# Optimization experiments

Measured on AMD Instinct MI355X. Metric: run time of the kernel, lower is better.

The kernel has to match this reference:

```python
import jax, jax.numpy as jnp
import numpy as np

GROUP_SIZE = 128  # in_features // scales.shape[1]


def setup_inputs() -> dict:
    key = jax.random.key(0)
    kA, kq, ks, kz, kb = jax.random.split(key, 5)
    M, K, N = 2048, 4096, 4096
    G = K // GROUP_SIZE  # 32 groups
    A = jax.random.normal(kA, (M, K), dtype=jnp.float32)
    # unpacked uint4 quantized weights, values in [0, 16)
    qweight = jax.random.randint(kq, (N, K), 0, 16, dtype=jnp.int32)
    # per-group scales (typical GPTQ magnitude) and zero-points (float, 'original' zeros_mode)
    scales = jax.random.uniform(ks, (N, G), dtype=jnp.float32) * 0.02
    zeros = jax.random.uniform(kz, (N, G), dtype=jnp.float32) * 15.0
    bias = jax.random.normal(kb, (N,), dtype=jnp.float32)
    return {"A": A, "qweight": qweight, "scales": scales, "zeros": zeros, "bias": bias}


def reference(A, qweight, scales, zeros, bias):
    # Dequant: W[n,k] = (q[n,k] - zeros[n, k//gs]) * scales[n, k//gs]
    N, K = qweight.shape
    gs = K // scales.shape[1]
    s = jnp.repeat(scales, gs, axis=1)  # [N, K]
    z = jnp.repeat(zeros, gs, axis=1)   # [N, K]
    W = (qweight.astype(A.dtype) - z) * s
    # out[m,n] = sum_k A[m,k] * W[n,k] + bias[n]
    return jnp.einsum("mk,nk->mn", A, W) + bias
```

## Files before the change

### kernel.cpp

```cpp
#include <hip/hip_runtime.h>
#include <cstdint>
#include <cstddef>

#define MM 2048
#define KK 4096
#define NN 4096
#define GG 32
#define BM 128
#define BN 128
#define BK 64

typedef _Float16 half8_t __attribute__((ext_vector_type(8)));
typedef _Float16 half4_t __attribute__((ext_vector_type(4)));
typedef float f32x4 __attribute__((ext_vector_type(4)));

__device__ __forceinline__ void load_lds16(const void* gptr, void* lptr) {
  __builtin_amdgcn_global_load_lds(
      (const __attribute__((address_space(1))) unsigned int*)gptr,
      (__attribute__((address_space(3))) unsigned int*)lptr, 16, 0, 0);
}

#define ACNT (MM * KK / 4)
__global__ void prep_kernel(const float* __restrict__ A, const int* __restrict__ q,
                            const float* __restrict__ scales, const float* __restrict__ zeros,
                            _Float16* __restrict__ Ah, _Float16* __restrict__ Wh) {
  const int i = blockIdx.x * blockDim.x + threadIdx.x;
  if (i < ACNT) {
    const float4 v = ((const float4*)A)[i];
    half4_t h;
    h[0] = (_Float16)v.x; h[1] = (_Float16)v.y; h[2] = (_Float16)v.z; h[3] = (_Float16)v.w;
    *(half4_t*)(Ah + 4 * (size_t)i) = h;
  } else {
    const int j = i - ACNT;
    const int e = j << 2;
    const int n = e >> 12;
    const int k = e & (KK - 1);
    const int g = k >> 7;
    const float sc = scales[(n << 5) + g];
    const float zp = zeros[(n << 5) + g];
    const float nzs = -zp * sc;
    const int4 qv = ((const int4*)q)[j];
    half4_t h;
    h[0] = (_Float16)fmaf((float)qv.x, sc, nzs);
    h[1] = (_Float16)fmaf((float)qv.y, sc, nzs);
    h[2] = (_Float16)fmaf((float)qv.z, sc, nzs);
    h[3] = (_Float16)fmaf((float)qv.w, sc, nzs);
    *(half4_t*)(Wh + (size_t)e) = h;
  }
}

template <bool FUSED>
__global__ __launch_bounds__(256, 2)
void gemm_kernel(const _Float16* __restrict__ Ah, const _Float16* __restrict__ Wh,
                 const float* __restrict__ Af, const int* __restrict__ qw,
                 const float* __restrict__ scales, const float* __restrict__ zeros,
                 const float* __restrict__ bias, float* __restrict__ out)
{
  __shared__ __align__(16) _Float16 sA[BM * BK];
  __shared__ __align__(16) _Float16 sB[BN * BK];

  const int tid = threadIdx.x;
  const int lane = tid & 63;
  const int wave = tid >> 6;
  const int wr = wave >> 1, wc = wave & 1;

  const int bid = blockIdx.x;
  const int xcd = bid & 7;
  const int slot = bid >> 3;
  const int mt = slot >> 2;
  const int nt = xcd * 4 + (slot & 3);
  const int m0 = mt * BM;
  const int n0 = nt * BN;

  const int lr = lane & 15, quad = lane >> 4;

  f32x4 acc[4][4];
#pragma unroll
  for (int i = 0; i < 4; ++i)
#pragma unroll
    for (int j = 0; j < 4; ++j) acc[i][j] = (f32x4){0.f, 0.f, 0.f, 0.f};

  const int srow = lane >> 3;
  const int scc = lane & 7;
  const int gchunk = scc ^ srow;

  const int frow = tid >> 4;
  const int fc4 = tid & 15;

  for (int kt = 0; kt < KK / BK; ++kt) {
    const int k0 = kt * BK;
    if constexpr (!FUSED) {
#pragma unroll
      for (int i = 0; i < 4; ++i) {
        const int c = i * 4 + wave;
        const int row = c * 8 + srow;
        load_lds16(Ah + (size_t)(m0 + row) * KK + k0 + gchunk * 8, (void*)&sA[c * 512]);
        load_lds16(Wh + (size_t)(n0 + row) * KK + k0 + gchunk * 8, (void*)&sB[c * 512]);
      }
    } else {
      const int g = k0 >> 7;
#pragma unroll
      for (int p = 0; p < 8; ++p) {
        const int row = p * 16 + frow;
        const int pc = (fc4 >> 1) ^ (row & 7);
        const int dst = row * 64 + pc * 8 + (fc4 & 1) * 4;
        const float4 avf = *(const float4*)&Af[(size_t)(m0 + row) * KK + k0 + fc4 * 4];
        half4_t ah;
        ah[0] = (_Float16)avf.x; ah[1] = (_Float16)avf.y;
        ah[2] = (_Float16)avf.z; ah[3] = (_Float16)avf.w;
        *(half4_t*)&sA[dst] = ah;
        const int n = n0 + row;
        const float sc = scales[(n << 5) + g];
        const float zp = zeros[(n << 5) + g];
        const float nzs = -zp * sc;
        const int4 qv = *(const int4*)&qw[(size_t)n * KK + k0 + fc4 * 4];
        half4_t bh;
        bh[0] = (_Float16)fmaf((float)qv.x, sc, nzs);
        bh[1] = (_Float16)fmaf((float)qv.y, sc, nzs);
        bh[2] = (_Float16)fmaf((float)qv.z, sc, nzs);
        bh[3] = (_Float16)fmaf((float)qv.w, sc, nzs);
        *(half4_t*)&sB[dst] = bh;
      }
    }
    __syncthreads();
#pragma unroll
    for (int ks = 0; ks < 2; ++ks) {
      half8_t a[4], b[4];
#pragma unroll
      for (int t = 0; t < 4; ++t) {
        const int rA = wr * 64 + t * 16 + lr;
        const int j = ks * 4 + quad;
        a[t] = *(const half8_t*)&sA[rA * 64 + ((j ^ (lr & 7)) * 8)];
        const int rB = wc * 64 + t * 16 + lr;
        b[t] = *(const half8_t*)&sB[rB * 64 + ((j ^ (lr & 7)) * 8)];
      }
#pragma unroll
      for (int mi = 0; mi < 4; ++mi)
#pragma unroll
        for (int ni = 0; ni < 4; ++ni)
          acc[mi][ni] = __builtin_amdgcn_mfma_f32_16x16x32_f16(a[mi], b[ni], acc[mi][ni], 0, 0, 0);
    }
    __syncthreads();
  }

#pragma unroll
  for (int ni = 0; ni < 4; ++ni) {
    const int n = n0 + wc * 64 + ni * 16 + lr;
    const float bv = bias[n];
#pragma unroll
    for (int mi = 0; mi < 4; ++mi) {
      const int mbase = m0 + wr * 64 + mi * 16 + quad * 4;
#pragma unroll
      for (int r = 0; r < 4; ++r)
        out[(size_t)(mbase + r) * NN + n] = acc[mi][ni][r] + bv;
    }
  }
}

extern "C" void kernel_launch(void* const* d_in, const int* in_sizes, int n_in,
                              void* d_out, int out_size, void* d_ws, size_t ws_size,
                              hipStream_t stream) {
  (void)in_sizes; (void)n_in; (void)out_size;
  const float* A      = (const float*)d_in[0];
  const int*   qw     = (const int*)d_in[1];
  const float* scales = (const float*)d_in[2];
  const float* zeros  = (const float*)d_in[3];
  const float* bias   = (const float*)d_in[4];
  float* out = (float*)d_out;

  const size_t needA = (size_t)MM * KK * sizeof(_Float16);
  const size_t needW = (size_t)NN * KK * sizeof(_Float16);

  dim3 grid(NN / BN * MM / BM);
  dim3 block(256);

  if (ws_size >= needA + needW) {
    _Float16* Ah = (_Float16*)d_ws;
    _Float16* Wh = (_Float16*)((char*)d_ws + needA);
    prep_kernel<<<((MM + NN) * KK / 4) / 256, 256, 0, stream>>>(A, qw, scales, zeros, Ah, Wh);
    gemm_kernel<false><<<grid, block, 0, stream>>>(Ah, Wh, A, qw, scales, zeros, bias, out);
  } else {
    gemm_kernel<true><<<grid, block, 0, stream>>>(nullptr, nullptr, A, qw, scales, zeros, bias, out);
  }
}
```

Measured before the change: 204.6 us.

## Add triple-buffered 8-wave GEMM with 128x256 tiles and interleaved LDS prefetch

Replaces the workspace GEMM path with a 512-thread, 8-wave kernel using 128x256 tiles and a three-stage LDS ring. Async global-to-LDS loads for tile t+2 are issued between the fragment reads and the MFMA phases, with explicit vmcnt waits, barriers and setprio, so memory traffic overlaps compute. The prep kernel also processes 8 elements per thread. The larger tiles cut redundant A/W reloads but raise LDS use (about 144KB per block) and register pressure, which may limit occupancy.

Result: no change. 207.7 us (+1.5%).

```diff
diff --git a/kernel.cpp b/kernel.cpp
--- a/kernel.cpp
+++ b/kernel.cpp
@@ -7,8 +7,9 @@
 #define NN 4096
 #define GG 32
 #define BM 128
-#define BN 128
+#define BN 256
 #define BK 64
+#define NTILES (KK / BK)
 
 typedef _Float16 half8_t __attribute__((ext_vector_type(8)));
 typedef _Float16 half4_t __attribute__((ext_vector_type(4)));
@@ -20,44 +21,170 @@
       (__attribute__((address_space(3))) unsigned int*)lptr, 16, 0, 0);
 }
 
-#define ACNT (MM * KK / 4)
+#define ACNT8 (MM * KK / 8)
 __global__ void prep_kernel(const float* __restrict__ A, const int* __restrict__ q,
                             const float* __restrict__ scales, const float* __restrict__ zeros,
                             _Float16* __restrict__ Ah, _Float16* __restrict__ Wh) {
   const int i = blockIdx.x * blockDim.x + threadIdx.x;
-  if (i < ACNT) {
-    const float4 v = ((const float4*)A)[i];
-    half4_t h;
-    h[0] = (_Float16)v.x; h[1] = (_Float16)v.y; h[2] = (_Float16)v.z; h[3] = (_Float16)v.w;
-    *(half4_t*)(Ah + 4 * (size_t)i) = h;
+  if (i < ACNT8) {
+    const float4 v0 = ((const float4*)A)[2 * (size_t)i];
+    const float4 v1 = ((const float4*)A)[2 * (size_t)i + 1];
+    half8_t h;
+    h[0] = (_Float16)v0.x; h[1] = (_Float16)v0.y; h[2] = (_Float16)v0.z; h[3] = (_Float16)v0.w;
+    h[4] = (_Float16)v1.x; h[5] = (_Float16)v1.y; h[6] = (_Float16)v1.z; h[7] = (_Float16)v1.w;
+    *(half8_t*)(Ah + 8 * (size_t)i) = h;
   } else {
-    const int j = i - ACNT;
-    const int e = j << 2;
+    const int j = i - ACNT8;
+    const int e = j << 3;
     const int n = e >> 12;
     const int k = e & (KK - 1);
     const int g = k >> 7;
     const float sc = scales[(n << 5) + g];
     const float zp = zeros[(n << 5) + g];
     const float nzs = -zp * sc;
-    const int4 qv = ((const int4*)q)[j];
-    half4_t h;
-    h[0] = (_Float16)fmaf((float)qv.x, sc, nzs);
-    h[1] = (_Float16)fmaf((float)qv.y, sc, nzs);
-    h[2] = (_Float16)fmaf((float)qv.z, sc, nzs);
-    h[3] = (_Float16)fmaf((float)qv.w, sc, nzs);
-    *(half4_t*)(Wh + (size_t)e) = h;
-  }
-}
-
-template <bool FUSED>
+    const int4 q0 = ((const int4*)q)[2 * (size_t)j];
+    const int4 q1 = ((const int4*)q)[2 * (size_t)j + 1];
+    half8_t h;
+    h[0] = (_Float16)fmaf((float)q0.x, sc, nzs);
+    h[1] = (_Float16)fmaf((float)q0.y, sc, nzs);
+    h[2] = (_Float16)fmaf((float)q0.z, sc, nzs);
+    h[3] = (_Float16)fmaf((float)q0.w, sc, nzs);
+    h[4] = (_Float16)fmaf((float)q1.x, sc, nzs);
+    h[5] = (_Float16)fmaf((float)q1.y, sc, nzs);
+    h[6] = (_Float16)fmaf((float)q1.z, sc, nzs);
+    h[7] = (_Float16)fmaf((float)q1.w, sc, nzs);
+    *(half8_t*)(Wh + (size_t)e) = h;
+  }
+}
+
+__global__ __launch_bounds__(512, 2)
+void gemm8_kernel(const _Float16* __restrict__ Ah, const _Float16* __restrict__ Wh,
+                  const float* __restrict__ bias, float* __restrict__ out)
+{
+  __shared__ __align__(16) _Float16 sA[3][BM * BK];
+  __shared__ __align__(16) _Float16 sB[3][BN * BK];
+
+  const int tid = threadIdx.x;
+  const int lane = tid & 63;
+  const int wave = tid >> 6;
+  const int wr = wave >> 2;
+  const int wc = wave & 3;
+  const int lr = lane & 15, quad = lane >> 4;
+
+  const int bid = blockIdx.x;
+  const int xcd = bid & 7;
+  const int slot = bid >> 3;
+  const int mt = slot >> 1;
+  const int nt = xcd * 2 + (slot & 1);
+  const int m0 = mt * BM;
+  const int n0 = nt * BN;
+
+  const int srow = lane >> 3, scc = lane & 7, gch = scc ^ srow;
+
+  f32x4 acc[4][4];
+#pragma unroll
+  for (int i = 0; i < 4; ++i)
+#pragma unroll
+    for (int j = 0; j < 4; ++j) acc[i][j] = (f32x4){0.f, 0.f, 0.f, 0.f};
+
+  auto stageA = [&](int t, int buf, int i) {
+    load_lds16(Ah + (size_t)(m0 + i * 64 + (wave << 3) + srow) * KK + t * BK + (gch << 3),
+               (void*)&sA[buf][(i * 64 + (wave << 3)) * BK]);
+  };
+  auto stageB = [&](int t, int buf, int i) {
+    load_lds16(Wh + (size_t)(n0 + i * 64 + (wave << 3) + srow) * KK + t * BK + (gch << 3),
+               (void*)&sB[buf][(i * 64 + (wave << 3)) * BK]);
+  };
+
+  stageB(0, 0, 0); stageB(0, 0, 1); stageA(0, 0, 0);
+  stageB(0, 0, 2); stageB(0, 0, 3); stageA(0, 0, 1);
+  stageB(1, 1, 0); stageB(1, 1, 1); stageA(1, 1, 0);
+  stageB(1, 1, 2); stageB(1, 1, 3); stageA(1, 1, 1);
+  asm volatile("s_waitcnt vmcnt(6)" ::: "memory");
+  __builtin_amdgcn_s_barrier();
+
+  int cur = 0, nb = 2;
+  for (int t = 0; t < NTILES; ++t) {
+    const _Float16* pA = sA[cur];
+    const _Float16* pB = sB[cur];
+    const bool st = (t < NTILES - 2);
+    half8_t a0[2][2], a1[2][2], b[4][2];
+
+#pragma unroll
+    for (int x = 0; x < 2; ++x) {
+      const _Float16* ba = &pA[(wr * 64 + x * 16 + lr) * BK];
+#pragma unroll
+      for (int ks = 0; ks < 2; ++ks)
+        a0[x][ks] = *(const half8_t*)&ba[((ks * 4 + quad) ^ (lr & 7)) * 8];
+    }
+#pragma unroll
+    for (int ni = 0; ni < 4; ++ni) {
+      const _Float16* bb = &pB[(wc * 64 + ni * 16 + lr) * BK];
+#pragma unroll
+      for (int ks = 0; ks < 2; ++ks)
+        b[ni][ks] = *(const half8_t*)&bb[((ks * 4 + quad) ^ (lr & 7)) * 8];
+    }
+    if (st) { stageB(t + 2, nb, 0); stageB(t + 2, nb, 1); stageA(t + 2, nb, 0); }
+    __builtin_amdgcn_sched_barrier(0);
+    __builtin_amdgcn_s_barrier();
+    __builtin_amdgcn_s_setprio(1);
+#pragma unroll
+    for (int x = 0; x < 2; ++x)
+#pragma unroll
+      for (int ni = 0; ni < 4; ++ni) {
+        acc[x][ni] = __builtin_amdgcn_mfma_f32_16x16x32_f16(a0[x][0], b[ni][0], acc[x][ni], 0, 0, 0);
+        acc[x][ni] = __builtin_amdgcn_mfma_f32_16x16x32_f16(a0[x][1], b[ni][1], acc[x][ni], 0, 0, 0);
+      }
+    __builtin_amdgcn_s_setprio(0);
+    __builtin_amdgcn_s_barrier();
+
+#pragma unroll
+    for (int x = 0; x < 2; ++x) {
+      const _Float16* ba = &pA[(wr * 64 + (x + 2) * 16 + lr) * BK];
+#pragma unroll
+      for (int ks = 0; ks < 2; ++ks)
+        a1[x][ks] = *(const half8_t*)&ba[((ks * 4 + quad) ^ (lr & 7)) * 8];
+    }
+    if (st) { stageB(t + 2, nb, 2); stageB(t + 2, nb, 3); stageA(t + 2, nb, 1); }
+    __builtin_amdgcn_sched_barrier(0);
+    __builtin_amdgcn_s_barrier();
+    __builtin_amdgcn_s_setprio(1);
+#pragma unroll
+    for (int x = 0; x < 2; ++x)
+#pragma unroll
+      for (int ni = 0; ni < 4; ++ni) {
+        acc[x + 2][ni] = __builtin_amdgcn_mfma_f32_16x16x32_f16(a1[x][0], b[ni][0], acc[x + 2][ni], 0, 0, 0);
+        acc[x + 2][ni] = __builtin_amdgcn_mfma_f32_16x16x32_f16(a1[x][1], b[ni][1], acc[x + 2][ni], 0, 0, 0);
+      }
+    __builtin_amdgcn_s_setprio(0);
+    if (t < NTILES - 2) asm volatile("s_waitcnt vmcnt(6)" ::: "memory");
+    else                asm volatile("s_waitcnt vmcnt(0)" ::: "memory");
+    __builtin_amdgcn_s_barrier();
+    cur = (cur == 2) ? 0 : cur + 1;
+    nb  = (nb  == 2) ? 0 : nb + 1;
+  }
+
+#pragma unroll
+  for (int ni = 0; ni < 4; ++ni) {
+    const int n = n0 + wc * 64 + ni * 16 + lr;
+    const float bv = bias[n];
+#pragma unroll
+    for (int mi = 0; mi < 4; ++mi) {
+      const int mbase = m0 + wr * 64 + mi * 16 + quad * 4;
+#pragma unroll
+      for (int r = 0; r < 4; ++r)
+        out[(size_t)(mbase + r) * NN + n] = acc[mi][ni][r] + bv;
+    }
+  }
+}
+
 __global__ __launch_bounds__(256, 2)
-void gemm_kernel(const _Float16* __restrict__ Ah, const _Float16* __restrict__ Wh,
-                 const float* __restrict__ Af, const int* __restrict__ qw,
-                 const float* __restrict__ scales, const float* __restrict__ zeros,
-                 const float* __restrict__ bias, float* __restrict__ out)
+void gemm_fused_kernel(const float* __restrict__ Af, const int* __restrict__ qw,
+                       const float* __restrict__ scales, const float* __restrict__ zeros,
+                       const float* __restrict__ bias, float* __restrict__ out)
 {
-  __shared__ __align__(16) _Float16 sA[BM * BK];
-  __shared__ __align__(16) _Float16 sB[BN * BK];
+  __shared__ __align__(16) _Float16 sA[128 * 64];
+  __shared__ __align__(16) _Float16 sB[128 * 64];
 
   const int tid = threadIdx.x;
   const int lane = tid & 63;
@@ -69,8 +196,8 @@
   const int slot = bid >> 3;
   const int mt = slot >> 2;
   const int nt = xcd * 4 + (slot & 3);
-  const int m0 = mt * BM;
-  const int n0 = nt * BN;
+  const int m0 = mt * 128;
+  const int n0 = nt * 128;
 
   const int lr = lane & 15, quad = lane >> 4;
 
@@ -79,48 +206,34 @@
   for (int i = 0; i < 4; ++i)
 #pragma unroll
     for (int j = 0; j < 4; ++j) acc[i][j] = (f32x4){0.f, 0.f, 0.f, 0.f};
-
-  const int srow = lane >> 3;
-  const int scc = lane & 7;
-  const int gchunk = scc ^ srow;
 
   const int frow = tid >> 4;
   const int fc4 = tid & 15;
 
-  for (int kt = 0; kt < KK / BK; ++kt) {
-    const int k0 = kt * BK;
-    if constexpr (!FUSED) {
-#pragma unroll
-      for (int i = 0; i < 4; ++i) {
-        const int c = i * 4 + wave;
-        const int row = c * 8 + srow;
-        load_lds16(Ah + (size_t)(m0 + row) * KK + k0 + gchunk * 8, (void*)&sA[c * 512]);
-        load_lds16(Wh + (size_t)(n0 + row) * KK + k0 + gchunk * 8, (void*)&sB[c * 512]);
-      }
-    } else {
-      const int g = k0 >> 7;
-#pragma unroll
-      for (int p = 0; p < 8; ++p) {
-        const int row = p * 16 + frow;
-        const int pc = (fc4 >> 1) ^ (row & 7);
-        const int dst = row * 64 + pc * 8 + (fc4 & 1) * 4;
-        const float4 avf = *(const float4*)&Af[(size_t)(m0 + row) * KK + k0 + fc4 * 4];
-        half4_t ah;
-        ah[0] = (_Float16)avf.x; ah[1] = (_Float16)avf.y;
-        ah[2] = (_Float16)avf.z; ah[3] = (_Float16)avf.w;
-        *(half4_t*)&sA[dst] = ah;
-        const int n = n0 + row;
-        const float sc = scales[(n << 5) + g];
-        const float zp = zeros[(n << 5) + g];
-        const float nzs = -zp * sc;
-        const int4 qv = *(const int4*)&qw[(size_t)n * KK + k0 + fc4 * 4];
-        half4_t bh;
-        bh[0] = (_Float16)fmaf((float)qv.x, sc, nzs);
-        bh[1] = (_Float16)fmaf((float)qv.y, sc, nzs);
-        bh[2] = (_Float16)fmaf((float)qv.z, sc, nzs);
-        bh[3] = (_Float16)fmaf((float)qv.w, sc, nzs);
-        *(half4_t*)&sB[dst] = bh;
-      }
+  for (int kt = 0; kt < KK / 64; ++kt) {
+    const int k0 = kt * 64;
+    const int g = k0 >> 7;
+#pragma unroll
+    for (int p = 0; p < 8; ++p) {
+      const int row = p * 16 + frow;
+      const int pc = (fc4 >> 1) ^ (row & 7);
+      const int dst = row * 64 + pc * 8 + (fc4 & 1) * 4;
+      const float4 avf = *(const float4*)&Af[(size_t)(m0 + row) * KK + k0 + fc4 * 4];
+      half4_t ah;
+      ah[0] = (_Float16)avf.x; ah[1] = (_Float16)avf.y;
+      ah[2] = (_Float16)avf.z; ah[3] = (_Float16)avf.w;
+      *(half4_t*)&sA[dst] = ah;
+      const int n = n0 + row;
+      const float sc = scales[(n << 5) + g];
+      const float zp = zeros[(n << 5) + g];
+      const float nzs = -zp * sc;
+      const int4 qv = *(const int4*)&qw[(size_t)n * KK + k0 + fc4 * 4];
+      half4_t bh;
+      bh[0] = (_Float16)fmaf((float)qv.x, sc, nzs);
+      bh[1] = (_Float16)fmaf((float)qv.y, sc, nzs);
+      bh[2] = (_Float16)fmaf((float)qv.z, sc, nzs);
+      bh[3] = (_Float16)fmaf((float)qv.w, sc, nzs);
+      *(half4_t*)&sB[dst] = bh;
     }
     __syncthreads();
 #pragma unroll
@@ -171,15 +284,12 @@
   const size_t needA = (size_t)MM * KK * sizeof(_Float16);
   const size_t needW = (size_t)NN * KK * sizeof(_Float16);
 
-  dim3 grid(NN / BN * MM / BM);
-  dim3 block(256);
-
   if (ws_size >= needA + needW) {
     _Float16* Ah = (_Float16*)d_ws;
     _Float16* Wh = (_Float16*)((char*)d_ws + needA);
-    prep_kernel<<<((MM + NN) * KK / 4) / 256, 256, 0, stream>>>(A, qw, scales, zeros, Ah, Wh);
-    gemm_kernel<false><<<grid, block, 0, stream>>>(Ah, Wh, A, qw, scales, zeros, bias, out);
+    prep_kernel<<<((MM + NN) * KK / 8) / 256, 256, 0, stream>>>(A, qw, scales, zeros, Ah, Wh);
+    gemm8_kernel<<<dim3(MM / BM * NN / BN), dim3(512), 0, stream>>>(Ah, Wh, bias, out);
   } else {
-    gemm_kernel<true><<<grid, block, 0, stream>>>(nullptr, nullptr, A, qw, scales, zeros, bias, out);
-  }
-}
+    gemm_fused_kernel<<<dim3(512), dim3(256), 0, stream>>>(A, qw, scales, zeros, bias, out);
+  }
+}
```

## Fuse dequant and fp32 conversion into a pipelined 128x256 triple-buffered GEMM

Applied to the files above, without the earlier changes.

Removes the separate prep kernel that wrote fp16 copies of A and W, and instead loads fp32 A and int32 weights directly into registers two tiles ahead. They are converted to fp16 and dequantized while being written into a triple-buffered LDS ring. The block tile grows to 128x256 with 512 threads and a single barrier per K tile, and MFMA issue is prioritized with setprio. This trades the extra HBM round trip of the prep pass for higher per-block global read volume of fp32/int32 data, plus heavy register and LDS usage (about 144KB).

Result: slower. 384.2 us (+87.7%).

```diff
diff --git a/kernel.cpp b/kernel.cpp
--- a/kernel.cpp
+++ b/kernel.cpp
@@ -7,72 +7,41 @@
 #define NN 4096
 #define GG 32
 #define BM 128
-#define BN 128
+#define BN 256
 #define BK 64
+#define NTILES (KK / BK)
 
 typedef _Float16 half8_t __attribute__((ext_vector_type(8)));
-typedef _Float16 half4_t __attribute__((ext_vector_type(4)));
 typedef float f32x4 __attribute__((ext_vector_type(4)));
 
-__device__ __forceinline__ void load_lds16(const void* gptr, void* lptr) {
-  __builtin_amdgcn_global_load_lds(
-      (const __attribute__((address_space(1))) unsigned int*)gptr,
-      (__attribute__((address_space(3))) unsigned int*)lptr, 16, 0, 0);
-}
-
-#define ACNT (MM * KK / 4)
-__global__ void prep_kernel(const float* __restrict__ A, const int* __restrict__ q,
-                            const float* __restrict__ scales, const float* __restrict__ zeros,
-                            _Float16* __restrict__ Ah, _Float16* __restrict__ Wh) {
-  const int i = blockIdx.x * blockDim.x + threadIdx.x;
-  if (i < ACNT) {
-    const float4 v = ((const float4*)A)[i];
-    half4_t h;
-    h[0] = (_Float16)v.x; h[1] = (_Float16)v.y; h[2] = (_Float16)v.z; h[3] = (_Float16)v.w;
-    *(half4_t*)(Ah + 4 * (size_t)i) = h;
-  } else {
-    const int j = i - ACNT;
-    const int e = j << 2;
-    const int n = e >> 12;
-    const int k = e & (KK - 1);
-    const int g = k >> 7;
-    const float sc = scales[(n << 5) + g];
-    const float zp = zeros[(n << 5) + g];
-    const float nzs = -zp * sc;
-    const int4 qv = ((const int4*)q)[j];
-    half4_t h;
-    h[0] = (_Float16)fmaf((float)qv.x, sc, nzs);
-    h[1] = (_Float16)fmaf((float)qv.y, sc, nzs);
-    h[2] = (_Float16)fmaf((float)qv.z, sc, nzs);
-    h[3] = (_Float16)fmaf((float)qv.w, sc, nzs);
-    *(half4_t*)(Wh + (size_t)e) = h;
-  }
-}
-
-template <bool FUSED>
-__global__ __launch_bounds__(256, 2)
-void gemm_kernel(const _Float16* __restrict__ Ah, const _Float16* __restrict__ Wh,
-                 const float* __restrict__ Af, const int* __restrict__ qw,
-                 const float* __restrict__ scales, const float* __restrict__ zeros,
-                 const float* __restrict__ bias, float* __restrict__ out)
+__global__ __launch_bounds__(512, 2)
+void gemm_fused13(const float* __restrict__ Af, const int* __restrict__ qw,
+                  const float* __restrict__ scales, const float* __restrict__ zeros,
+                  const float* __restrict__ bias, float* __restrict__ out)
 {
-  __shared__ __align__(16) _Float16 sA[BM * BK];
-  __shared__ __align__(16) _Float16 sB[BN * BK];
+  __shared__ __align__(16) _Float16 sA[3][BM * BK];
+  __shared__ __align__(16) _Float16 sB[3][BN * BK];
 
   const int tid = threadIdx.x;
   const int lane = tid & 63;
   const int wave = tid >> 6;
-  const int wr = wave >> 1, wc = wave & 1;
+  const int wr = wave >> 2;
+  const int wc = wave & 3;
+  const int lr = lane & 15, quad = lane >> 4;
 
   const int bid = blockIdx.x;
   const int xcd = bid & 7;
   const int slot = bid >> 3;
-  const int mt = slot >> 2;
-  const int nt = xcd * 4 + (slot & 3);
+  const int mt = slot >> 1;
+  const int nt = xcd * 2 + (slot & 1);
   const int m0 = mt * BM;
   const int n0 = nt * BN;
 
-  const int lr = lane & 15, quad = lane >> 4;
+  const int arow = tid >> 2, aquad = tid & 3;
+  const int brow = tid >> 1, bhalf = tid & 1;
+  const size_t aBase = (size_t)(m0 + arow) * KK;
+  const size_t bBase = (size_t)(n0 + brow) * KK;
+  const int szBase = (n0 + brow) << 5;
 
   f32x4 acc[4][4];
 #pragma unroll
@@ -80,68 +49,113 @@
 #pragma unroll
     for (int j = 0; j < 4; ++j) acc[i][j] = (f32x4){0.f, 0.f, 0.f, 0.f};
 
-  const int srow = lane >> 3;
-  const int scc = lane & 7;
-  const int gchunk = scc ^ srow;
+  float4 aR0[4], aR1[4];
+  int4   bR0[8], bR1[8];
+  float  sc0, nz0, sc1, nz1;
 
-  const int frow = tid >> 4;
-  const int fc4 = tid & 15;
+#define LOADSET(T, aR, bR, scR, nzR)                                            \
+  do {                                                                          \
+    const int k0_ = (T) * BK;                                                   \
+    _Pragma("unroll")                                                           \
+    for (int j = 0; j < 4; ++j)                                                 \
+      aR[j] = *(const float4*)&Af[aBase + k0_ + aquad * 16 + j * 4];            \
+    _Pragma("unroll")                                                           \
+    for (int i = 0; i < 8; ++i)                                                 \
+      bR[i] = *(const int4*)&qw[bBase + k0_ + bhalf * 32 + i * 4];              \
+    const int g_ = (T) >> 1;                                                    \
+    scR = scales[szBase + g_];                                                  \
+    nzR = -zeros[szBase + g_] * scR;                                            \
+  } while (0)
 
-  for (int kt = 0; kt < KK / BK; ++kt) {
-    const int k0 = kt * BK;
-    if constexpr (!FUSED) {
-#pragma unroll
-      for (int i = 0; i < 4; ++i) {
-        const int c = i * 4 + wave;
-        const int row = c * 8 + srow;
-        load_lds16(Ah + (size_t)(m0 + row) * KK + k0 + gchunk * 8, (void*)&sA[c * 512]);
-        load_lds16(Wh + (size_t)(n0 + row) * KK + k0 + gchunk * 8, (void*)&sB[c * 512]);
-      }
-    } else {
-      const int g = k0 >> 7;
-#pragma unroll
-      for (int p = 0; p < 8; ++p) {
-        const int row = p * 16 + frow;
-        const int pc = (fc4 >> 1) ^ (row & 7);
-        const int dst = row * 64 + pc * 8 + (fc4 & 1) * 4;
-        const float4 avf = *(const float4*)&Af[(size_t)(m0 + row) * KK + k0 + fc4 * 4];
-        half4_t ah;
-        ah[0] = (_Float16)avf.x; ah[1] = (_Float16)avf.y;
-        ah[2] = (_Float16)avf.z; ah[3] = (_Float16)avf.w;
-        *(half4_t*)&sA[dst] = ah;
-        const int n = n0 + row;
-        const float sc = scales[(n << 5) + g];
-        const float zp = zeros[(n << 5) + g];
-        const float nzs = -zp * sc;
-        const int4 qv = *(const int4*)&qw[(size_t)n * KK + k0 + fc4 * 4];
-        half4_t bh;
-        bh[0] = (_Float16)fmaf((float)qv.x, sc, nzs);
-        bh[1] = (_Float16)fmaf((float)qv.y, sc, nzs);
-        bh[2] = (_Float16)fmaf((float)qv.z, sc, nzs);
-        bh[3] = (_Float16)fmaf((float)qv.w, sc, nzs);
-        *(half4_t*)&sB[dst] = bh;
-      }
-    }
-    __syncthreads();
-#pragma unroll
-    for (int ks = 0; ks < 2; ++ks) {
-      half8_t a[4], b[4];
-#pragma unroll
-      for (int t = 0; t < 4; ++t) {
-        const int rA = wr * 64 + t * 16 + lr;
-        const int j = ks * 4 + quad;
-        a[t] = *(const half8_t*)&sA[rA * 64 + ((j ^ (lr & 7)) * 8)];
-        const int rB = wc * 64 + t * 16 + lr;
-        b[t] = *(const half8_t*)&sB[rB * 64 + ((j ^ (lr & 7)) * 8)];
-      }
-#pragma unroll
-      for (int mi = 0; mi < 4; ++mi)
-#pragma unroll
-        for (int ni = 0; ni < 4; ++ni)
-          acc[mi][ni] = __builtin_amdgcn_mfma_f32_16x16x32_f16(a[mi], b[ni], acc[mi][ni], 0, 0, 0);
-    }
-    __syncthreads();
+#define WRITESET(BUF, aR, bR, scR, nzR)                                         \
+  do {                                                                          \
+    _Pragma("unroll")                                                           \
+    for (int j = 0; j < 2; ++j) {                                               \
+      const float4 v0 = aR[2 * j], v1 = aR[2 * j + 1];                          \
+      half8_t h;                                                                \
+      h[0] = (_Float16)v0.x; h[1] = (_Float16)v0.y;                             \
+      h[2] = (_Float16)v0.z; h[3] = (_Float16)v0.w;                             \
+      h[4] = (_Float16)v1.x; h[5] = (_Float16)v1.y;                             \
+      h[6] = (_Float16)v1.z; h[7] = (_Float16)v1.w;                             \
+      *(half8_t*)&sA[BUF][arow * BK + (((aquad * 2 + j) ^ (arow & 7)) * 8)] = h;\
+    }                                                                           \
+    _Pragma("unroll")                                                           \
+    for (int j = 0; j < 4; ++j) {                                               \
+      const int4 q0 = bR[2 * j], q1 = bR[2 * j + 1];                            \
+      half8_t h;                                                                \
+      h[0] = (_Float16)fmaf((float)q0.x, scR, nzR);                             \
+      h[1] = (_Float16)fmaf((float)q0.y, scR, nzR);                             \
+      h[2] = (_Float16)fmaf((float)q0.z, scR, nzR);                             \
+      h[3] = (_Float16)fmaf((float)q0.w, scR, nzR);                             \
+      h[4] = (_Float16)fmaf((float)q1.x, scR, nzR);                             \
+      h[5] = (_Float16)fmaf((float)q1.y, scR, nzR);                             \
+      h[6] = (_Float16)fmaf((float)q1.z, scR, nzR);                             \
+      h[7] = (_Float16)fmaf((float)q1.w, scR, nzR);                             \
+      *(half8_t*)&sB[BUF][brow * BK + (((bhalf * 4 + j) ^ (brow & 7)) * 8)] = h;\
+    }                                                                           \
+  } while (0)
+
+#define TILE(T, aL, bL, scL, nzL, aC, bC, scC, nzC)                             \
+  do {                                                                          \
+    const _Float16* pA = sA[cur];                                               \
+    const _Float16* pB = sB[cur];                                               \
+    half8_t fa0[2][2], fa1[2][2], fb[4][2];                                     \
+    _Pragma("unroll")                                                           \
+    for (int x = 0; x < 2; ++x) {                                               \
+      const _Float16* ba = &pA[(wr * 64 + x * 16 + lr) * BK];                   \
+      _Pragma("unroll")                                                         \
+      for (int ks = 0; ks < 2; ++ks)                                            \
+        fa0[x][ks] = *(const half8_t*)&ba[((ks * 4 + quad) ^ (lr & 7)) * 8];    \
+    }                                                                           \
+    _Pragma("unroll")                                                           \
+    for (int ni = 0; ni < 4; ++ni) {                                            \
+      const _Float16* bb = &pB[(wc * 64 + ni * 16 + lr) * BK];                  \
+      _Pragma("unroll")                                                         \
+      for (int ks = 0; ks < 2; ++ks)                                            \
+        fb[ni][ks] = *(const half8_t*)&bb[((ks * 4 + quad) ^ (lr & 7)) * 8];    \
+    }                                                                           \
+    _Pragma("unroll")                                                           \
+    for (int x = 0; x < 2; ++x) {                                               \
+      const _Float16* ba = &pA[(wr * 64 + (x + 2) * 16 + lr) * BK];             \
+      _Pragma("unroll")                                                         \
+      for (int ks = 0; ks < 2; ++ks)                                            \
+        fa1[x][ks] = *(const half8_t*)&ba[((ks * 4 + quad) ^ (lr & 7)) * 8];    \
+    }                                                                           \
+    if ((T) + 2 < NTILES) LOADSET((T) + 2, aL, bL, scL, nzL);                   \
+    __builtin_amdgcn_sched_barrier(0);                                          \
+    if ((T) + 1 < NTILES) WRITESET(nxt, aC, bC, scC, nzC);                      \
+    __builtin_amdgcn_s_setprio(1);                                              \
+    _Pragma("unroll")                                                           \
+    for (int x = 0; x < 2; ++x)                                                 \
+      _Pragma("unroll")                                                         \
+      for (int ni = 0; ni < 4; ++ni) {                                          \
+        acc[x][ni] = __builtin_amdgcn_mfma_f32_16x16x32_f16(fa0[x][0], fb[ni][0], acc[x][ni], 0, 0, 0);         \
+        acc[x][ni] = __builtin_amdgcn_mfma_f32_16x16x32_f16(fa0[x][1], fb[ni][1], acc[x][ni], 0, 0, 0);         \
+        acc[x + 2][ni] = __builtin_amdgcn_mfma_f32_16x16x32_f16(fa1[x][0], fb[ni][0], acc[x + 2][ni], 0, 0, 0); \
+        acc[x + 2][ni] = __builtin_amdgcn_mfma_f32_16x16x32_f16(fa1[x][1], fb[ni][1], acc[x + 2][ni], 0, 0, 0); \
+      }                                                                         \
+    __builtin_amdgcn_s_setprio(0);                                              \
+    asm volatile("s_waitcnt lgkmcnt(0)" ::: "memory");                          \
+    __builtin_amdgcn_s_barrier();                                               \
+    cur = (cur == 2) ? 0 : cur + 1;                                             \
+    nxt = (nxt == 2) ? 0 : nxt + 1;                                             \
+  } while (0)
+
+  LOADSET(0, aR0, bR0, sc0, nz0);
+  WRITESET(0, aR0, bR0, sc0, nz0);
+  LOADSET(1, aR1, bR1, sc1, nz1);
+  asm volatile("s_waitcnt lgkmcnt(0)" ::: "memory");
+  __builtin_amdgcn_s_barrier();
+
+  int cur = 0, nxt = 1;
+  for (int t = 0; t < NTILES; t += 2) {
+    TILE(t,     aR0, bR0, sc0, nz0, aR1, bR1, sc1, nz1);
+    TILE(t + 1, aR1, bR1, sc1, nz1, aR0, bR0, sc0, nz0);
   }
+
+#undef TILE
+#undef WRITESET
+#undef LOADSET
 
 #pragma unroll
   for (int ni = 0; ni < 4; ++ni) {
@@ -160,7 +174,7 @@
 extern "C" void kernel_launch(void* const* d_in, const int* in_sizes, int n_in,
                               void* d_out, int out_size, void* d_ws, size_t ws_size,
                               hipStream_t stream) {
-  (void)in_sizes; (void)n_in; (void)out_size;
+  (void)in_sizes; (void)n_in; (void)out_size; (void)d_ws; (void)ws_size;
   const float* A      = (const float*)d_in[0];
   const int*   qw     = (const int*)d_in[1];
   const float* scales = (const float*)d_in[2];
@@ -168,18 +182,6 @@
   const float* bias   = (const float*)d_in[4];
   float* out = (float*)d_out;
 
-  const size_t needA = (size_t)MM * KK * sizeof(_Float16);
-  const size_t needW = (size_t)NN * KK * sizeof(_Float16);
-
-  dim3 grid(NN / BN * MM / BM);
-  dim3 block(256);
-
-  if (ws_size >= needA + needW) {
-    _Float16* Ah = (_Float16*)d_ws;
-    _Float16* Wh = (_Float16*)((char*)d_ws + needA);
-    prep_kernel<<<((MM + NN) * KK / 4) / 256, 256, 0, stream>>>(A, qw, scales, zeros, Ah, Wh);
-    gemm_kernel<false><<<grid, block, 0, stream>>>(Ah, Wh, A, qw, scales, zeros, bias, out);
-  } else {
-    gemm_kernel<true><<<grid, block, 0, stream>>>(nullptr, nullptr, A, qw, scales, zeros, bias, out);
-  }
+  gemm_fused13<<<dim3(MM / BM * NN / BN), dim3(512), 0, stream>>>(
+      A, qw, scales, zeros, bias, out);
 }
```
